# Performance work log

Hardware: AMD Instinct MI355X
Metric: run time of the kernel (lower is better)

## Reference

```python
import jax, jax.numpy as jnp
import numpy as np

NUM_PATCHES = 16
FILTER_SIZE = 4
IN_CHANNELS = 64
OUT_CHANNELS = 256
BATCH = 64


def setup_inputs() -> dict:
    key = jax.random.key(0)
    k1, k2 = jax.random.split(key)
    D = NUM_PATCHES * FILTER_SIZE
    x = jax.random.normal(k1, (BATCH, IN_CHANNELS, D, D), dtype=jnp.float32)
    w = jax.random.normal(
        k2,
        (OUT_CHANNELS, IN_CHANNELS, NUM_PATCHES, NUM_PATCHES, FILTER_SIZE ** 2),
        dtype=jnp.float32,
    )
    return {"x": x, "w": w}


def reference(x, w):
    # x: (N, C, D, D) with D = P*f ; w: (O, C, P, P, f^2)
    N, C, D, _ = x.shape
    O, _, P, _, f2 = w.shape
    f = int(round(f2 ** 0.5))
    # non-overlapping unfold: (N,C,P,f,P,f) -> (N,C,P,P,f,f) -> (N,C,P,P,f^2)
    patches = x.reshape(N, C, P, f, P, f).transpose(0, 1, 2, 4, 3, 5).reshape(N, C, P, P, f2)
    # locally-connected contraction over in_channels and filter elements
    y = jnp.einsum('ncpqf,ocpqf->nopq', patches, w)
    scale = 1.0 / jnp.sqrt(jnp.asarray(f2 * C, dtype=x.dtype))
    return jax.nn.relu(y * scale)
```

## Files before the change

kernel.cpp:

```cpp
#include <hip/hip_runtime.h>


typedef short bf16x8 __attribute__((ext_vector_type(8)));
typedef float f32x4  __attribute__((ext_vector_type(4)));

__device__ __forceinline__ short f2bf(float f) {
    union { float f; unsigned u; } v; v.f = f;
    return (short)((v.u + 0x7FFFu + ((v.u >> 16) & 1u)) >> 16);
}

__device__ __forceinline__ bf16x8 pack8(f32x4 a, f32x4 b) {
    bf16x8 r;
    r[0] = f2bf(a[0]); r[1] = f2bf(a[1]); r[2] = f2bf(a[2]); r[3] = f2bf(a[3]);
    r[4] = f2bf(b[0]); r[5] = f2bf(b[1]); r[6] = f2bf(b[2]); r[7] = f2bf(b[3]);
    return r;
}

__device__ __forceinline__ void gload16(const void* g, void* l) {
    __builtin_amdgcn_global_load_lds(
        (const __attribute__((address_space(1))) void*)g,
        (__attribute__((address_space(3))) void*)l, 16, 0, 0);
}

__global__ __launch_bounds__(512)
void locblock_fused(const float* __restrict__ x, const float* __restrict__ w,
                    float* __restrict__ out) {
    __shared__ __align__(16) char smem[131072];

    const int hw = blockIdx.x;
    const int lb = (hw & 7) * 32 + (hw >> 3);
    const int p  = lb >> 4;
    const int q4 = (lb >> 2) & 3;
    const int oq = lb & 3;

    const int tid  = (int)threadIdx.x;
    const int lane = tid & 63;
    const int wv   = tid >> 6;
    const int l15  = lane & 15;
    const int kq   = lane >> 4;
    const int qiw  = wv >> 1;
    const int ow   = wv & 1;

    const float* xsrc[4];
#pragma unroll
    for (int j = 0; j < 4; ++j) {
        const int id = j * 512 + tid;
        const int n = id >> 5, s = id & 31;
        const int u = s ^ (n & 15);
        xsrc[j] = x + (size_t)n * 262144u + (size_t)(u >> 4) * 4096u
                    + (size_t)(4 * p + ((u >> 2) & 3)) * 64u
                    + (size_t)(q4 * 16 + (u & 3) * 4);
    }
    const float* wsrc[4];
#pragma unroll
    for (int j = 0; j < 4; ++j) {
        const int id = j * 512 + tid;
        const int o = id >> 5, s = id & 31;
        const int u = s ^ (o & 15);
        wsrc[j] = w + (size_t)(oq * 64 + o) * 262144u + (size_t)(u >> 4) * 4096u
                    + (size_t)p * 256u + (size_t)(q4 * 64) + (size_t)((u & 15) * 4);
    }

    int aoff[4][2], boff[2][2];
    {
        const int coff = kq >> 1, fr0 = (kq & 1) * 2;
#pragma unroll
        for (int mf = 0; mf < 4; ++mf) {
            const int n = mf * 16 + l15;
#pragma unroll
            for (int d = 0; d < 2; ++d)
                aoff[mf][d] = n * 512
                    + (coff * 16 + (((fr0 + d) * 4 + qiw) ^ l15)) * 16;
        }
#pragma unroll
        for (int nf = 0; nf < 2; ++nf) {
            const int o = ow * 32 + nf * 16 + l15;
#pragma unroll
            for (int e = 0; e < 2; ++e)
                boff[nf][e] = 32768 + o * 512
                    + (coff * 16 + ((qiw * 4 + (kq & 1) * 2 + e) ^ l15)) * 16;
        }
    }

    f32x4 acc[4][2];
#pragma unroll
    for (int mf = 0; mf < 4; ++mf)
#pragma unroll
        for (int nf = 0; nf < 2; ++nf)
            acc[mf][nf] = (f32x4){0.f, 0.f, 0.f, 0.f};

    auto stage = [&](int t) {
        char* base = smem + (size_t)(t & 1) * 65536u;
        const size_t toff = (size_t)t * 8192u;
#pragma unroll
        for (int j = 0; j < 4; ++j)
            gload16(xsrc[j] + toff, base + j * 8192 + tid * 16);
#pragma unroll
        for (int j = 0; j < 4; ++j)
            gload16(wsrc[j] + toff, base + 32768 + j * 8192 + tid * 16);
    };

    auto compute = [&](int t) {
        const char* Lb = smem + (size_t)(t & 1) * 65536u;
        bf16x8 av[4], bv[2];
#pragma unroll
        for (int mf = 0; mf < 4; ++mf)
            av[mf] = pack8(*(const f32x4*)(Lb + aoff[mf][0]),
                           *(const f32x4*)(Lb + aoff[mf][1]));
#pragma unroll
        for (int nf = 0; nf < 2; ++nf)
            bv[nf] = pack8(*(const f32x4*)(Lb + boff[nf][0]),
                           *(const f32x4*)(Lb + boff[nf][1]));
#pragma unroll
        for (int mf = 0; mf < 4; ++mf)
#pragma unroll
            for (int nf = 0; nf < 2; ++nf)
                acc[mf][nf] = __builtin_amdgcn_mfma_f32_16x16x32_bf16(
                    av[mf], bv[nf], acc[mf][nf], 0, 0, 0);
    };

    stage(0);
    stage(1);
#pragma unroll 1
    for (int t = 0; t < 30; ++t) {
        asm volatile("s_waitcnt vmcnt(8)" ::: "memory");
        __builtin_amdgcn_s_barrier();
        compute(t);
        asm volatile("s_waitcnt lgkmcnt(0)" ::: "memory");
        __builtin_amdgcn_s_barrier();
        stage(t + 2);
    }
    asm volatile("s_waitcnt vmcnt(8)" ::: "memory");
    __builtin_amdgcn_s_barrier();
    compute(30);
    asm volatile("s_waitcnt vmcnt(0)" ::: "memory");
    __builtin_amdgcn_s_barrier();
    compute(31);

    __syncthreads();

    float* T = (float*)smem;
    const float scale = 0.03125f;
#pragma unroll
    for (int mf = 0; mf < 4; ++mf)
#pragma unroll
        for (int nf = 0; nf < 2; ++nf) {
            const int o  = ow * 32 + nf * 16 + l15;
            const int n0 = mf * 16 + kq * 4;
            f32x4 r;
#pragma unroll
            for (int j = 0; j < 4; ++j)
                r[j] = fmaxf(acc[mf][nf][j] * scale, 0.0f);
            *(f32x4*)(T + (size_t)(qiw * 64 + o) * 72u + n0) = r;
        }
    __syncthreads();

#pragma unroll
    for (int i = 0; i < 8; ++i) {
        const int item = i * 512 + tid;
        const int n = item >> 6, o = item & 63;
        f32x4 r;
#pragma unroll
        for (int s = 0; s < 4; ++s)
            r[s] = T[(size_t)(s * 64 + o) * 72u + n];
        *(f32x4*)(out + (size_t)n * 65536u + (size_t)(oq * 64 + o) * 256u
                      + (size_t)(p * 16 + q4 * 4)) = r;
    }
}

extern "C" void kernel_launch(void* const* d_in, const int* in_sizes, int n_in,
                              void* d_out, int out_size, void* d_ws, size_t ws_size,
                              hipStream_t stream) {
    const float* x = (const float*)d_in[0];
    const float* w = (const float*)d_in[1];
    float* out = (float*)d_out;
    locblock_fused<<<dim3(256), dim3(512), 0, stream>>>(x, w, out);
}
```

Baseline: 86.41 us.

## Use fp16 16x16x16 MFMA with four-stage single-barrier LDS pipeline

Switches the MFMA from bf16 16x16x32 to f16 16x16x16, using a simpler fp32-to-fp16 conversion. Tiles are halved to one channel per stage, and the double buffer becomes a four-buffer ring with three stages in flight, so only one barrier per iteration is needed and the next stage is issued before compute. This aims to overlap global-to-LDS loads with MFMA work and cut conversion and synchronisation overhead. The cost is twice as many iterations and fp16 range and precision limits on the inputs.

```diff
diff --git a/kernel.cpp b/kernel.cpp
--- a/kernel.cpp
+++ b/kernel.cpp
@@ -1,25 +1,20 @@
 #include <hip/hip_runtime.h>
 
 
-typedef short bf16x8 __attribute__((ext_vector_type(8)));
-typedef float f32x4  __attribute__((ext_vector_type(4)));
-
-__device__ __forceinline__ short f2bf(float f) {
-    union { float f; unsigned u; } v; v.f = f;
-    return (short)((v.u + 0x7FFFu + ((v.u >> 16) & 1u)) >> 16);
-}
-
-__device__ __forceinline__ bf16x8 pack8(f32x4 a, f32x4 b) {
-    bf16x8 r;
-    r[0] = f2bf(a[0]); r[1] = f2bf(a[1]); r[2] = f2bf(a[2]); r[3] = f2bf(a[3]);
-    r[4] = f2bf(b[0]); r[5] = f2bf(b[1]); r[6] = f2bf(b[2]); r[7] = f2bf(b[3]);
-    return r;
-}
+typedef float    f32x4 __attribute__((ext_vector_type(4)));
+typedef _Float16 f16x4 __attribute__((ext_vector_type(4)));
 
 __device__ __forceinline__ void gload16(const void* g, void* l) {
     __builtin_amdgcn_global_load_lds(
         (const __attribute__((address_space(1))) void*)g,
         (__attribute__((address_space(3))) void*)l, 16, 0, 0);
+}
+
+__device__ __forceinline__ f16x4 cvt4(f32x4 v) {
+    f16x4 r;
+    r[0] = (_Float16)v[0]; r[1] = (_Float16)v[1];
+    r[2] = (_Float16)v[2]; r[3] = (_Float16)v[3];
+    return r;
 }
 
 __global__ __launch_bounds__(512)
@@ -35,52 +30,41 @@
 
     const int tid  = (int)threadIdx.x;
     const int lane = tid & 63;
-    const int wv   = tid >> 6;
     const int l15  = lane & 15;
     const int kq   = lane >> 4;
+    const int wv   = tid >> 6;
     const int qiw  = wv >> 1;
     const int ow   = wv & 1;
 
-    const float* xsrc[4];
+    const float* xsrc[2];
 #pragma unroll
-    for (int j = 0; j < 4; ++j) {
+    for (int j = 0; j < 2; ++j) {
         const int id = j * 512 + tid;
-        const int n = id >> 5, s = id & 31;
+        const int n = id >> 4, s = id & 15;
         const int u = s ^ (n & 15);
-        xsrc[j] = x + (size_t)n * 262144u + (size_t)(u >> 4) * 4096u
-                    + (size_t)(4 * p + ((u >> 2) & 3)) * 64u
+        xsrc[j] = x + (size_t)n * 262144u
+                    + (size_t)(4 * p + (u >> 2)) * 64u
                     + (size_t)(q4 * 16 + (u & 3) * 4);
     }
-    const float* wsrc[4];
+    const float* wsrc[2];
 #pragma unroll
-    for (int j = 0; j < 4; ++j) {
+    for (int j = 0; j < 2; ++j) {
         const int id = j * 512 + tid;
-        const int o = id >> 5, s = id & 31;
+        const int o = id >> 4, s = id & 15;
         const int u = s ^ (o & 15);
-        wsrc[j] = w + (size_t)(oq * 64 + o) * 262144u + (size_t)(u >> 4) * 4096u
-                    + (size_t)p * 256u + (size_t)(q4 * 64) + (size_t)((u & 15) * 4);
+        wsrc[j] = w + (size_t)(oq * 64 + o) * 262144u
+                    + (size_t)p * 256u + (size_t)(q4 * 64)
+                    + (size_t)((u >> 2) * 16 + (u & 3) * 4);
     }
 
-    int aoff[4][2], boff[2][2];
-    {
-        const int coff = kq >> 1, fr0 = (kq & 1) * 2;
+    int aoff[4], boff[2];
 #pragma unroll
-        for (int mf = 0; mf < 4; ++mf) {
-            const int n = mf * 16 + l15;
+    for (int mf = 0; mf < 4; ++mf)
+        aoff[mf] = (mf * 16 + l15) * 256 + (((kq * 4 + qiw) ^ l15) * 16);
 #pragma unroll
-            for (int d = 0; d < 2; ++d)
-                aoff[mf][d] = n * 512
-                    + (coff * 16 + (((fr0 + d) * 4 + qiw) ^ l15)) * 16;
-        }
-#pragma unroll
-        for (int nf = 0; nf < 2; ++nf) {
-            const int o = ow * 32 + nf * 16 + l15;
-#pragma unroll
-            for (int e = 0; e < 2; ++e)
-                boff[nf][e] = 32768 + o * 512
-                    + (coff * 16 + ((qiw * 4 + (kq & 1) * 2 + e) ^ l15)) * 16;
-        }
-    }
+    for (int nf = 0; nf < 2; ++nf)
+        boff[nf] = 16384 + (ow * 32 + nf * 16 + l15) * 256
+                 + (((qiw * 4 + kq) ^ l15) * 16);
 
     f32x4 acc[4][2];
 #pragma unroll
@@ -89,53 +73,53 @@
         for (int nf = 0; nf < 2; ++nf)
             acc[mf][nf] = (f32x4){0.f, 0.f, 0.f, 0.f};
 
-    auto stage = [&](int t) {
-        char* base = smem + (size_t)(t & 1) * 65536u;
-        const size_t toff = (size_t)t * 8192u;
+    auto stage = [&](int c) {
+        char* base = smem + (size_t)(c & 3) * 32768u;
+        const size_t coff = (size_t)c * 4096u;
 #pragma unroll
-        for (int j = 0; j < 4; ++j)
-            gload16(xsrc[j] + toff, base + j * 8192 + tid * 16);
+        for (int j = 0; j < 2; ++j)
+            gload16(xsrc[j] + coff, base + j * 8192 + tid * 16);
 #pragma unroll
-        for (int j = 0; j < 4; ++j)
-            gload16(wsrc[j] + toff, base + 32768 + j * 8192 + tid * 16);
+        for (int j = 0; j < 2; ++j)
+            gload16(wsrc[j] + coff, base + 16384 + j * 8192 + tid * 16);
     };
 
-    auto compute = [&](int t) {
-        const char* Lb = smem + (size_t)(t & 1) * 65536u;
-        bf16x8 av[4], bv[2];
+    auto compute = [&](int c) {
+        const char* Lb = smem + (size_t)(c & 3) * 32768u;
+        f16x4 av[4], bv[2];
 #pragma unroll
         for (int mf = 0; mf < 4; ++mf)
-            av[mf] = pack8(*(const f32x4*)(Lb + aoff[mf][0]),
-                           *(const f32x4*)(Lb + aoff[mf][1]));
+            av[mf] = cvt4(*(const f32x4*)(Lb + aoff[mf]));
 #pragma unroll
         for (int nf = 0; nf < 2; ++nf)
-            bv[nf] = pack8(*(const f32x4*)(Lb + boff[nf][0]),
-                           *(const f32x4*)(Lb + boff[nf][1]));
+            bv[nf] = cvt4(*(const f32x4*)(Lb + boff[nf]));
 #pragma unroll
         for (int mf = 0; mf < 4; ++mf)
 #pragma unroll
             for (int nf = 0; nf < 2; ++nf)
-                acc[mf][nf] = __builtin_amdgcn_mfma_f32_16x16x32_bf16(
+                acc[mf][nf] = __builtin_amdgcn_mfma_f32_16x16x16f16(
                     av[mf], bv[nf], acc[mf][nf], 0, 0, 0);
     };
 
     stage(0);
     stage(1);
+    stage(2);
 #pragma unroll 1
-    for (int t = 0; t < 30; ++t) {
+    for (int t = 0; t < 61; ++t) {
         asm volatile("s_waitcnt vmcnt(8)" ::: "memory");
         __builtin_amdgcn_s_barrier();
+        stage(t + 3);
         compute(t);
-        asm volatile("s_waitcnt lgkmcnt(0)" ::: "memory");
-        __builtin_amdgcn_s_barrier();
-        stage(t + 2);
     }
     asm volatile("s_waitcnt vmcnt(8)" ::: "memory");
     __builtin_amdgcn_s_barrier();
-    compute(30);
+    compute(61);
+    asm volatile("s_waitcnt vmcnt(4)" ::: "memory");
+    __builtin_amdgcn_s_barrier();
+    compute(62);
     asm volatile("s_waitcnt vmcnt(0)" ::: "memory");
     __builtin_amdgcn_s_barrier();
-    compute(31);
+    compute(63);
 
     __syncthreads();
 
```

New measurement: 85.41 us, median of 2. Within noise of the previous version (-1.1%).
